# Kernel tuning notes

Measured on AMD Instinct MI355X. Metric: run time of the kernel, lower is better.

The kernel has to match this reference:

```python
import jax, jax.numpy as jnp
import numpy as np

DIM = 768
HEADS = 12
HD = DIM // HEADS  # 64
WIN = 14
N = WIN * WIN  # 196
MLP_HID = 3072
EPS = 1e-6
SCALE = HD ** -0.5


def _ln(x, g, b):
    m = jnp.mean(x, axis=-1, keepdims=True)
    v = jnp.mean(jnp.square(x - m), axis=-1, keepdims=True)
    return (x - m) * jax.lax.rsqrt(v + EPS) * g + b


def _rel_table(rel):
    coords = jnp.arange(WIN)[:, None] - jnp.arange(WIN)[None, :] + (WIN - 1)
    return rel[coords]


def _window_partition(x, ws):
    B, H, W, C = x.shape
    pad_h = (ws - H % ws) % ws
    pad_w = (ws - W % ws) % ws
    x = jnp.pad(x, ((0, 0), (0, pad_h), (0, pad_w), (0, 0)))
    Hp, Wp = H + pad_h, W + pad_w
    x = x.reshape(B, Hp // ws, ws, Wp // ws, ws, C)
    win = x.transpose(0, 1, 3, 2, 4, 5).reshape(-1, ws, ws, C)
    return win, (Hp, Wp)


def _window_unpartition(win, ws, pad_hw, hw):
    Hp, Wp = pad_hw
    H, W = hw
    B = win.shape[0] // (Hp * Wp // ws // ws)
    x = win.reshape(B, Hp // ws, Wp // ws, ws, ws, -1)
    x = x.transpose(0, 1, 3, 2, 4, 5).reshape(B, Hp, Wp, -1)
    return x[:, :H, :W, :]


def _attention(x, qkv_w, qkv_b, proj_w, proj_b, rel_pos_h, rel_pos_w):
    Bw = x.shape[0]
    qkv = x.reshape(Bw, N, DIM) @ qkv_w + qkv_b  # (Bw, N, 3*DIM)
    qkv = qkv.reshape(Bw, N, 3, HEADS, HD).transpose(2, 0, 3, 1, 4)
    qkv = qkv.reshape(3, Bw * HEADS, N, HD)
    q, k, v = qkv[0], qkv[1], qkv[2]
    attn = jnp.einsum('bnd,bmd->bnm', q * SCALE, k)  # (Bw*H, N, N)
    Rh = _rel_table(rel_pos_h)
    Rw = _rel_table(rel_pos_w)
    r_q = q.reshape(-1, WIN, WIN, HD)
    rel_h = jnp.einsum('bhwc,hkc->bhwk', r_q, Rh)
    rel_w = jnp.einsum('bhwc,wkc->bhwk', r_q, Rw)
    attn = (attn.reshape(-1, WIN, WIN, WIN, WIN)
            + rel_h[:, :, :, :, None]
            + rel_w[:, :, :, None, :]).reshape(-1, N, N)
    attn = jax.nn.softmax(attn, axis=-1)
    out = jnp.einsum('bnm,bmd->bnd', attn, v)
    out = out.reshape(Bw, HEADS, WIN, WIN, HD).transpose(0, 2, 3, 1, 4)
    out = out.reshape(Bw, WIN, WIN, DIM)
    return out @ proj_w + proj_b


def setup_inputs() -> dict:
    key = jax.random.key(0)
    ks = jax.random.split(key, 10)
    s = 0.02
    return {
        'x': jax.random.normal(ks[0], (2, 64, 64, DIM), jnp.float32),
        'ln1_g': jnp.ones((DIM,), jnp.float32),
        'ln1_b': jnp.zeros((DIM,), jnp.float32),
        'qkv_w': jax.random.normal(ks[1], (DIM, 3 * DIM), jnp.float32) * s,
        'qkv_b': jax.random.normal(ks[2], (3 * DIM,), jnp.float32) * s,
        'proj_w': jax.random.normal(ks[3], (DIM, DIM), jnp.float32) * s,
        'proj_b': jax.random.normal(ks[4], (DIM,), jnp.float32) * s,
        'rel_pos_h': jax.random.normal(ks[5], (2 * WIN - 1, HD), jnp.float32) * s,
        'rel_pos_w': jax.random.normal(ks[6], (2 * WIN - 1, HD), jnp.float32) * s,
        'ln2_g': jnp.ones((DIM,), jnp.float32),
        'ln2_b': jnp.zeros((DIM,), jnp.float32),
        'fc1_w': jax.random.normal(ks[7], (DIM, MLP_HID), jnp.float32) * s,
        'fc1_b': jnp.zeros((MLP_HID,), jnp.float32),
        'fc2_w': jax.random.normal(ks[8], (MLP_HID, DIM), jnp.float32) * s,
        'fc2_b': jnp.zeros((DIM,), jnp.float32),
    }


def reference(x, ln1_g, ln1_b, qkv_w, qkv_b, proj_w, proj_b,
              rel_pos_h, rel_pos_w, ln2_g, ln2_b, fc1_w, fc1_b, fc2_w, fc2_b):
    B, H, W, _ = x.shape
    shortcut = x
    h = _ln(x, ln1_g, ln1_b)
    win, pad_hw = _window_partition(h, WIN)
    win = _attention(win, qkv_w, qkv_b, proj_w, proj_b, rel_pos_h, rel_pos_w)
    h = _window_unpartition(win, WIN, pad_hw, (H, W))
    x = shortcut + h  # drop_path prob 0 -> identity
    h = _ln(x, ln2_g, ln2_b)
    h = jax.nn.gelu(h @ fc1_w + fc1_b, approximate=False) @ fc2_w + fc2_b
    return x + h
```

## Files before the change

kernel.cpp:

```cpp
#include <hip/hip_runtime.h>
#include <hip/hip_bf16.h>
#include <math.h>


#define DIMC 768
#define HEADS 12
#define WIN 14
#define NTOK 196
#define NWIN 50
#define MROWS 9800
#define YROWS 8192
#define MLP_HID 3072

using bf16x8 = __attribute__((ext_vector_type(8))) short;
using f32x4  = __attribute__((ext_vector_type(4))) float;

__device__ __forceinline__ float bf2f(unsigned short u) {
    return __uint_as_float(((unsigned)u) << 16);
}
__device__ __forceinline__ unsigned short f2bf(float f) {
    unsigned u = __float_as_uint(f);
    unsigned r = (u + 0x7fffu + ((u >> 16) & 1u)) >> 16;
    return (unsigned short)r;
}
__device__ __forceinline__ void gl2lds16(const unsigned short* g, unsigned short* l) {
    __builtin_amdgcn_global_load_lds(
        (const __attribute__((address_space(1))) void*)g,
        (__attribute__((address_space(3))) void*)l, 16, 0, 0);
}

__global__ __launch_bounds__(256) void transpose_w(
        const float* __restrict__ W, unsigned short* __restrict__ Wt,
        int K, int N) {
    __shared__ float t[64][65];
    int k0 = blockIdx.y << 6, n0 = blockIdx.x << 6;
    int tn = threadIdx.x & 63;
    int tk = threadIdx.x >> 6;
    #pragma unroll
    for (int r = 0; r < 16; r++) {
        int k = tk + r * 4;
        t[k][tn] = W[(size_t)(k0 + k) * N + n0 + tn];
    }
    __syncthreads();
    #pragma unroll
    for (int r = 0; r < 16; r++) {
        int n = tk + r * 4;
        Wt[(size_t)(n0 + n) * K + k0 + tn] = f2bf(t[tn][n]);
    }
}

__global__ __launch_bounds__(256) void ln1_win_kernel(
        const float* __restrict__ x, const float* __restrict__ g,
        const float* __restrict__ b, unsigned short* __restrict__ h1) {
    int tid = threadIdx.x;
    int row = blockIdx.x * 4 + (tid >> 6);
    int lane = tid & 63;
    if (row >= MROWS) return;
    int w = row / NTOK, t = row % NTOK;
    int bi = w / 25, wr = w % 25;
    int gy = (wr / 5) * WIN + t / WIN;
    int gx = (wr % 5) * WIN + t % WIN;
    unsigned short* out = h1 + (size_t)row * DIMC;
    if (gy >= 64 || gx >= 64) {
        #pragma unroll
        for (int j = 0; j < 12; j++) out[lane + 64 * j] = 0;
        return;
    }
    const float* xr = x + ((size_t)((bi * 64 + gy) * 64 + gx)) * DIMC;
    float v[12], s = 0.f;
    #pragma unroll
    for (int j = 0; j < 12; j++) { v[j] = xr[lane + 64 * j]; s += v[j]; }
    #pragma unroll
    for (int o = 32; o > 0; o >>= 1) s += __shfl_xor(s, o);
    float mean = s * (1.f / 768.f);
    float q = 0.f;
    #pragma unroll
    for (int j = 0; j < 12; j++) { float d = v[j] - mean; q += d * d; }
    #pragma unroll
    for (int o = 32; o > 0; o >>= 1) q += __shfl_xor(q, o);
    float inv = rsqrtf(q * (1.f / 768.f) + 1e-6f);
    #pragma unroll
    for (int j = 0; j < 12; j++) {
        int c = lane + 64 * j;
        out[c] = f2bf((v[j] - mean) * inv * g[c] + b[c]);
    }
}

__global__ __launch_bounds__(256) void ln2_kernel(
        const float* __restrict__ y, const float* __restrict__ g,
        const float* __restrict__ b, unsigned short* __restrict__ h2) {
    int tid = threadIdx.x;
    int row = blockIdx.x * 4 + (tid >> 6);
    int lane = tid & 63;
    const float* xr = y + (size_t)row * DIMC;
    float v[12], s = 0.f;
    #pragma unroll
    for (int j = 0; j < 12; j++) { v[j] = xr[lane + 64 * j]; s += v[j]; }
    #pragma unroll
    for (int o = 32; o > 0; o >>= 1) s += __shfl_xor(s, o);
    float mean = s * (1.f / 768.f);
    float q = 0.f;
    #pragma unroll
    for (int j = 0; j < 12; j++) { float d = v[j] - mean; q += d * d; }
    #pragma unroll
    for (int o = 32; o > 0; o >>= 1) q += __shfl_xor(q, o);
    float inv = rsqrtf(q * (1.f / 768.f) + 1e-6f);
    unsigned short* out = h2 + (size_t)row * DIMC;
    #pragma unroll
    for (int j = 0; j < 12; j++) {
        int c = lane + 64 * j;
        out[c] = f2bf((v[j] - mean) * inv * g[c] + b[c]);
    }
}

__global__ __launch_bounds__(256) void build_aug(
        const unsigned short* __restrict__ qkvb,
        const float* __restrict__ relph, const float* __restrict__ relpw,
        unsigned short* __restrict__ Aaug, unsigned short* __restrict__ Vt) {
    __shared__ unsigned short qs[208 * 72];
    __shared__ unsigned short rt[64 * 72];
    int tid = threadIdx.x;
    int bh = blockIdx.x, w = bh / HEADS, head = bh % HEADS;
    int lane = tid & 63, wave = tid >> 6;
    int l15 = lane & 15, q4 = lane >> 4, q8 = q4 * 8;
    size_t base = (size_t)w * NTOK * 2304 + head * 64;
    unsigned short* ab = Aaug + (size_t)bh * 256 * 96;

    for (int e = tid; e < 196 * 8; e += 256) {
        int t = e >> 3, s8 = (e & 7) * 8;
        bf16x8 qv = *(const bf16x8*)&qkvb[base + (size_t)t * 2304 + s8];
        *(bf16x8*)&qs[t * 72 + s8] = qv;
        *(bf16x8*)&ab[t * 96 + s8] = qv;
    }
    for (int e = tid; e < 12 * 8; e += 256) {
        bf16x8 z = {};
        *(bf16x8*)&qs[(196 + (e >> 3)) * 72 + (e & 7) * 8] = z;
    }
    for (int e = tid; e < 64 * 8; e += 256) {
        int r = e >> 3, s8 = (e & 7) * 8;
        bf16x8 ov = {};
        if (r < 54) {
            const float* src = (r < 27 ? relph + (size_t)r * 64
                                       : relpw + (size_t)(r - 27) * 64) + s8;
            #pragma unroll
            for (int jj = 0; jj < 8; jj++) ov[jj] = (short)f2bf(src[jj]);
        }
        *(bf16x8*)&rt[r * 72 + s8] = ov;
    }
    for (int e = tid; e < 60 * 12; e += 256) {
        bf16x8 z = {};
        *(bf16x8*)&ab[(size_t)(196 + e / 12) * 96 + (e % 12) * 8] = z;
    }
    for (int e = tid; e < 196; e += 256) {
        ab[e * 96 + 92] = 0; ab[e * 96 + 93] = 0;
        ab[e * 96 + 94] = 0; ab[e * 96 + 95] = 0;
    }
    __syncthreads();

    #pragma unroll
    for (int t = 0; t < 4; t++) {
        int it = wave * 4 + t;
        if (it >= 13) break;
        bf16x8 a0 = *(bf16x8*)&qs[(it * 16 + l15) * 72 + q8];
        bf16x8 a1 = *(bf16x8*)&qs[(it * 16 + l15) * 72 + 32 + q8];
        #pragma unroll
        for (int rt4 = 0; rt4 < 4; rt4++) {
            bf16x8 b0 = *(bf16x8*)&rt[(rt4 * 16 + l15) * 72 + q8];
            bf16x8 b1 = *(bf16x8*)&rt[(rt4 * 16 + l15) * 72 + 32 + q8];
            f32x4 d4 = {};
            d4 = __builtin_amdgcn_mfma_f32_16x16x32_bf16(a0, b0, d4, 0, 0, 0);
            d4 = __builtin_amdgcn_mfma_f32_16x16x32_bf16(a1, b1, d4, 0, 0, 0);
            int rcol = rt4 * 16 + l15;
            #pragma unroll
            for (int r = 0; r < 4; r++) {
                int i = it * 16 + q4 * 4 + r;
                if (i < 196 && rcol < 54) {
                    if (rcol < 27) {
                        int c = 13 + i / 14 - rcol;
                        if (c >= 0 && c < 14) ab[i * 96 + 64 + c] = f2bf(d4[r]);
                    } else {
                        int c = 13 + i % 14 - (rcol - 27);
                        if (c >= 0 && c < 14) ab[i * 96 + 78 + c] = f2bf(d4[r]);
                    }
                }
            }
        }
    }

    unsigned short* vtb = Vt + (size_t)bh * 64 * 224;
    for (int e = tid; e < 196 * 8; e += 256) {
        int j = e >> 3, dg = (e & 7) * 8;
        bf16x8 vv = *(const bf16x8*)&qkvb[base + 1536 + (size_t)j * 2304 + dg];
        #pragma unroll
        for (int k = 0; k < 8; k++)
            vtb[(size_t)(dg + k) * 224 + j] = (unsigned short)vv[k];
    }
    for (int e = tid; e < 64 * 28; e += 256)
        vtb[(size_t)(e / 28) * 224 + 196 + (e % 28)] = 0;
}

__global__ __launch_bounds__(256) void attn_mfma(
        const unsigned short* __restrict__ qkvb,
        const unsigned short* __restrict__ Aaug,
        const unsigned short* __restrict__ Vt,
        unsigned short* __restrict__ out) {
    __shared__ unsigned short Kls[208 * 96];
    __shared__ unsigned short Pls[4][64 * 40];
    int tid = threadIdx.x;
    int bh = blockIdx.x, w = bh / HEADS, head = bh % HEADS;
    int wave = tid >> 6, lane = tid & 63;
    int l15 = lane & 15, q4 = lane >> 4, q8 = q4 * 8;
    size_t kbase = (size_t)w * NTOK * 2304 + head * 64 + 768;
    for (int e = tid; e < 196 * 8; e += 256) {
        int t = e >> 3, s8 = (e & 7) * 8;
        bf16x8 kv = *(const bf16x8*)&qkvb[kbase + (size_t)t * 2304 + s8];
        bf16x8 ko;
        #pragma unroll
        for (int jj = 0; jj < 8; jj++)
            ko[jj] = (short)f2bf(bf2f((unsigned short)kv[jj]) * 0.125f);
        *(bf16x8*)&Kls[t * 96 + s8] = ko;
    }
    bf16x8 z8 = {};
    for (int e = tid; e < 208 * 4; e += 256)
        *(bf16x8*)&Kls[(e >> 2) * 96 + 64 + (e & 3) * 8] = z8;
    for (int e = tid; e < 12 * 8; e += 256)
        *(bf16x8*)&Kls[(196 + (e >> 3)) * 96 + (e & 7) * 8] = z8;
    __syncthreads();
    for (int e = tid; e < 196; e += 256) {
        Kls[e * 96 + 64 + e / WIN] = 0x3F80;
        Kls[e * 96 + 78 + e % WIN] = 0x3F80;
    }
    bf16x8 af[4][3];
    const unsigned short* abse = Aaug + (size_t)bh * 256 * 96;
    #pragma unroll
    for (int it = 0; it < 4; it++)
        #pragma unroll
        for (int c = 0; c < 3; c++)
            af[it][c] = *(const bf16x8*)&abse[(size_t)(wave * 64 + it * 16 + l15) * 96 + c * 32 + q8];
    __syncthreads();

    const unsigned short* vtb = Vt + (size_t)bh * 64 * 224;
    f32x4 o[4][4] = {};
    float lacc[4][4] = {{0.f}};
    bf16x8 bv[4];
    #pragma unroll
    for (int dt = 0; dt < 4; dt++)
        bv[dt] = *(const bf16x8*)&vtb[(dt * 16 + l15) * 224 + q8];

    for (int jp = 0; jp < 7; jp++) {
        f32x4 s[4][2] = {};
        #pragma unroll
        for (int half = 0; half < 2; half++) {
            int jt = jp * 2 + half;
            if (jt < 13) {
                #pragma unroll
                for (int c = 0; c < 3; c++) {
                    bf16x8 bk = *(bf16x8*)&Kls[(jt * 16 + l15) * 96 + c * 32 + q8];
                    #pragma unroll
                    for (int it = 0; it < 4; it++)
                        s[it][half] = __builtin_amdgcn_mfma_f32_16x16x32_bf16(
                            af[it][c], bk, s[it][half], 0, 0, 0);
                }
            }
        }
        __syncthreads();
        #pragma unroll
        for (int half = 0; half < 2; half++) {
            int jt = jp * 2 + half;
            bool valid = (jt < 13) && (jt * 16 + l15) < 196;
            #pragma unroll
            for (int it = 0; it < 4; it++)
                #pragma unroll
                for (int r = 0; r < 4; r++) {
                    float p = valid ? __expf(s[it][half][r]) : 0.f;
                    unsigned short pb = f2bf(p);
                    lacc[it][r] += bf2f(pb);
                    Pls[wave][(it * 16 + q4 * 4 + r) * 40 + half * 16 + l15] = pb;
                }
        }
        __syncthreads();
        bf16x8 ap[4];
        #pragma unroll
        for (int it = 0; it < 4; it++)
            ap[it] = *(bf16x8*)&Pls[wave][(it * 16 + l15) * 40 + q8];
        bf16x8 bvn[4];
        if (jp < 6) {
            #pragma unroll
            for (int dt = 0; dt < 4; dt++)
                bvn[dt] = *(const bf16x8*)&vtb[(dt * 16 + l15) * 224 + (jp + 1) * 32 + q8];
        }
        #pragma unroll
        for (int dt = 0; dt < 4; dt++)
            #pragma unroll
            for (int it = 0; it < 4; it++)
                o[it][dt] = __builtin_amdgcn_mfma_f32_16x16x32_bf16(
                    ap[it], bv[dt], o[it][dt], 0, 0, 0);
        if (jp < 6) {
            #pragma unroll
            for (int dt = 0; dt < 4; dt++) bv[dt] = bvn[dt];
        }
    }
    #pragma unroll
    for (int it = 0; it < 4; it++)
        #pragma unroll
        for (int r = 0; r < 4; r++) {
            float v = lacc[it][r];
            v += __shfl_xor(v, 1); v += __shfl_xor(v, 2);
            v += __shfl_xor(v, 4); v += __shfl_xor(v, 8);
            lacc[it][r] = 1.f / v;
        }
    #pragma unroll
    for (int it = 0; it < 4; it++) {
        int i0 = wave * 64 + it * 16 + q4 * 4;
        #pragma unroll
        for (int r = 0; r < 4; r++) {
            if (i0 + r < 196) {
                size_t rowb = (size_t)(w * NTOK + i0 + r) * DIMC + head * 64;
                #pragma unroll
                for (int dt = 0; dt < 4; dt++)
                    out[rowb + dt * 16 + l15] = f2bf(o[it][dt][r] * lacc[it][r]);
            }
        }
    }
}

template <int EPI>
__global__ __launch_bounds__(256) void mgemm(
        const unsigned short* __restrict__ A, const unsigned short* __restrict__ Bt,
        const float* __restrict__ bias, void* __restrict__ Cout,
        const float* __restrict__ resid, int M, int Nn, int K) {
    __shared__ unsigned short As[128 * 32];
    __shared__ unsigned short Bs[128 * 32];
    int tid = threadIdx.x;
    int lane = tid & 63, wave = tid >> 6;
    int l15 = lane & 15, q8 = (lane >> 4) * 8;
    int m0 = blockIdx.y << 7, n0 = blockIdx.x << 7;
    int wm = (wave >> 1) * 64, wn = (wave & 1) * 64;
    int srow0 = wave * 32 + (lane >> 2);
    int srow1 = srow0 + 16;
    int sseg = (lane & 3) * 8;
    int rmA0 = m0 + srow0; if (rmA0 >= M) rmA0 = M - 1;
    int rmA1 = m0 + srow1; if (rmA1 >= M) rmA1 = M - 1;
    const unsigned short* gA0 = A + (size_t)rmA0 * K + sseg;
    const unsigned short* gA1 = A + (size_t)rmA1 * K + sseg;
    const unsigned short* gB0 = Bt + (size_t)(n0 + srow0) * K + sseg;
    const unsigned short* gB1 = Bt + (size_t)(n0 + srow1) * K + sseg;
    unsigned short* lA0 = As + wave * 1024 + lane * 8;
    unsigned short* lA1 = lA0 + 512;
    unsigned short* lB0 = Bs + wave * 1024 + lane * 8;
    unsigned short* lB1 = lB0 + 512;
    f32x4 acc[4][4] = {};
    for (int k0 = 0; k0 < K; k0 += 32) {
        gl2lds16(gA0 + k0, lA0);
        gl2lds16(gA1 + k0, lA1);
        gl2lds16(gB0 + k0, lB0);
        gl2lds16(gB1 + k0, lB1);
        __syncthreads();
        bf16x8 bfr[4];
        #pragma unroll
        for (int ni = 0; ni < 4; ni++)
            bfr[ni] = *(bf16x8*)&Bs[(wn + ni * 16 + l15) * 32 + q8];
        #pragma unroll
        for (int mi = 0; mi < 4; mi++) {
            bf16x8 afr = *(bf16x8*)&As[(wm + mi * 16 + l15) * 32 + q8];
            #pragma unroll
            for (int ni = 0; ni < 4; ni++)
                acc[mi][ni] = __builtin_amdgcn_mfma_f32_16x16x32_bf16(
                    afr, bfr[ni], acc[mi][ni], 0, 0, 0);
        }
        __syncthreads();
    }
    int q4r = (lane >> 4) * 4;
    #pragma unroll
    for (int mi = 0; mi < 4; mi++) {
        #pragma unroll
        for (int r = 0; r < 4; r++) {
            int row = m0 + wm + mi * 16 + q4r + r;
            if (row >= M) continue;
            if (EPI == 2) {
                int w = row / NTOK, t = row % NTOK;
                int bi = w / 25, wr = w % 25;
                int gy = (wr / 5) * WIN + t / WIN;
                int gx = (wr % 5) * WIN + t % WIN;
                if (gy >= 64 || gx >= 64) continue;
                size_t orow = ((size_t)((bi * 64 + gy) * 64 + gx)) * DIMC;
                #pragma unroll
                for (int ni = 0; ni < 4; ni++) {
                    int col = n0 + wn + ni * 16 + l15;
                    float v = acc[mi][ni][r] + bias[col];
                    ((float*)Cout)[orow + col] = resid[orow + col] + v;
                }
            } else {
                #pragma unroll
                for (int ni = 0; ni < 4; ni++) {
                    int col = n0 + wn + ni * 16 + l15;
                    float v = acc[mi][ni][r] + bias[col];
                    if (EPI == 0) {
                        ((unsigned short*)Cout)[(size_t)row * Nn + col] = f2bf(v);
                    } else if (EPI == 1) {
                        v = 0.5f * v * (1.f + erff(v * 0.70710678118654752f));
                        ((unsigned short*)Cout)[(size_t)row * Nn + col] = f2bf(v);
                    } else {
                        ((float*)Cout)[(size_t)row * Nn + col] =
                            resid[(size_t)row * Nn + col] + v;
                    }
                }
            }
        }
    }
}

extern "C" void kernel_launch(void* const* d_in, const int* in_sizes, int n_in,
                              void* d_out, int out_size, void* d_ws, size_t ws_size,
                              hipStream_t stream) {
    const float* x      = (const float*)d_in[0];
    const float* ln1_g  = (const float*)d_in[1];
    const float* ln1_b  = (const float*)d_in[2];
    const float* qkv_w  = (const float*)d_in[3];
    const float* qkv_b  = (const float*)d_in[4];
    const float* proj_w = (const float*)d_in[5];
    const float* proj_b = (const float*)d_in[6];
    const float* rel_h  = (const float*)d_in[7];
    const float* rel_w  = (const float*)d_in[8];
    const float* ln2_g  = (const float*)d_in[9];
    const float* ln2_b  = (const float*)d_in[10];
    const float* fc1_w  = (const float*)d_in[11];
    const float* fc1_b  = (const float*)d_in[12];
    const float* fc2_w  = (const float*)d_in[13];
    const float* fc2_b  = (const float*)d_in[14];
    float* out = (float*)d_out;
    char* ws = (char*)d_ws;

    unsigned short* wt_qkv  = (unsigned short*)(ws);
    unsigned short* wt_proj = (unsigned short*)(ws + 3538944);
    unsigned short* wt_fc1  = (unsigned short*)(ws + 4718592);
    unsigned short* wt_fc2  = (unsigned short*)(ws + 9437184);
    unsigned short* qkvb    = (unsigned short*)(ws + 14155776);
    float*          yb      = (float*)        (ws + 14155776);
    unsigned short* h2      = (unsigned short*)(ws + 39321600);
    unsigned short* h1      = (unsigned short*)(ws + 59314176);
    unsigned short* attn_o  = h1;
    unsigned short* zb      = h1;
    unsigned short* Aaug    = (unsigned short*)(ws + 74366976);
    unsigned short* Vt      = (unsigned short*)(ws + 103858176);

    transpose_w<<<dim3(36, 12), 256, 0, stream>>>(qkv_w,  wt_qkv,  768, 2304);
    transpose_w<<<dim3(12, 12), 256, 0, stream>>>(proj_w, wt_proj, 768, 768);
    transpose_w<<<dim3(48, 12), 256, 0, stream>>>(fc1_w,  wt_fc1,  768, 3072);
    transpose_w<<<dim3(12, 48), 256, 0, stream>>>(fc2_w,  wt_fc2,  3072, 768);

    ln1_win_kernel<<<(MROWS + 3) / 4, 256, 0, stream>>>(x, ln1_g, ln1_b, h1);

    mgemm<0><<<dim3(18, 77), 256, 0, stream>>>(
        h1, wt_qkv, qkv_b, qkvb, nullptr, MROWS, 2304, DIMC);

    build_aug<<<NWIN * HEADS, 256, 0, stream>>>(qkvb, rel_h, rel_w, Aaug, Vt);

    attn_mfma<<<NWIN * HEADS, 256, 0, stream>>>(qkvb, Aaug, Vt, attn_o);

    mgemm<2><<<dim3(6, 77), 256, 0, stream>>>(
        attn_o, wt_proj, proj_b, yb, x, MROWS, DIMC, DIMC);

    ln2_kernel<<<YROWS / 4, 256, 0, stream>>>(yb, ln2_g, ln2_b, h2);

    mgemm<1><<<dim3(24, 64), 256, 0, stream>>>(
        h2, wt_fc1, fc1_b, zb, nullptr, YROWS, MLP_HID, DIMC);

    mgemm<3><<<dim3(6, 64), 256, 0, stream>>>(
        zb, wt_fc2, fc2_b, out, yb, YROWS, DIMC, MLP_HID);
}
```

Baseline: 474.4 us.

## Add grouped block swizzle and narrower N tiles for projection and fc2 GEMMs

The GEMM kernel now takes a 1D grid and remaps block IDs into groups of 8 M-tiles, so neighbouring blocks share A rows and B columns in L2. The N tile width becomes a template parameter. The projection and fc2 GEMMs use 64-wide N tiles, which doubles their block count from 462/384 to 924/768 and fills more CUs. The trade-off is less reuse per block and more redundant A loads for the narrow-tile GEMMs.

```diff
diff --git a/kernel.cpp b/kernel.cpp
--- a/kernel.cpp
+++ b/kernel.cpp
@@ -324,18 +324,28 @@
     }
 }
 
-template <int EPI>
+template <int EPI, int BN>
 __global__ __launch_bounds__(256) void mgemm(
         const unsigned short* __restrict__ A, const unsigned short* __restrict__ Bt,
         const float* __restrict__ bias, void* __restrict__ Cout,
-        const float* __restrict__ resid, int M, int Nn, int K) {
+        const float* __restrict__ resid, int M, int Nn, int K,
+        int nbx, int nby) {
+    const int NI = BN / 32;
     __shared__ unsigned short As[128 * 32];
-    __shared__ unsigned short Bs[128 * 32];
+    __shared__ unsigned short Bs[BN * 32];
     int tid = threadIdx.x;
     int lane = tid & 63, wave = tid >> 6;
     int l15 = lane & 15, q8 = (lane >> 4) * 8;
-    int m0 = blockIdx.y << 7, n0 = blockIdx.x << 7;
-    int wm = (wave >> 1) * 64, wn = (wave & 1) * 64;
+    int id = blockIdx.x;
+    int per = nbx * 8;
+    int s = id / per;
+    int rem = id - s * per;
+    int rmax = nby - s * 8; if (rmax > 8) rmax = 8;
+    int bx = rem / rmax;
+    int r_ = rem - bx * rmax;
+    int by = s * 8 + r_;
+    int m0 = by << 7, n0 = bx * BN;
+    int wm = (wave >> 1) * 64, wn = (wave & 1) * (BN / 2);
     int srow0 = wave * 32 + (lane >> 2);
     int srow1 = srow0 + 16;
     int sseg = (lane & 3) * 8;
@@ -343,28 +353,29 @@
     int rmA1 = m0 + srow1; if (rmA1 >= M) rmA1 = M - 1;
     const unsigned short* gA0 = A + (size_t)rmA0 * K + sseg;
     const unsigned short* gA1 = A + (size_t)rmA1 * K + sseg;
-    const unsigned short* gB0 = Bt + (size_t)(n0 + srow0) * K + sseg;
-    const unsigned short* gB1 = Bt + (size_t)(n0 + srow1) * K + sseg;
     unsigned short* lA0 = As + wave * 1024 + lane * 8;
     unsigned short* lA1 = lA0 + 512;
-    unsigned short* lB0 = Bs + wave * 1024 + lane * 8;
+    int browB = (BN == 128) ? srow0 : (wave * 16 + (lane >> 2));
+    const unsigned short* gB0 = Bt + (size_t)(n0 + browB) * K + sseg;
+    const unsigned short* gB1 = Bt + (size_t)(n0 + srow1) * K + sseg;
+    unsigned short* lB0 = Bs + ((BN == 128) ? wave * 1024 : wave * 512) + lane * 8;
     unsigned short* lB1 = lB0 + 512;
-    f32x4 acc[4][4] = {};
+    f32x4 acc[4][NI] = {};
     for (int k0 = 0; k0 < K; k0 += 32) {
         gl2lds16(gA0 + k0, lA0);
         gl2lds16(gA1 + k0, lA1);
         gl2lds16(gB0 + k0, lB0);
-        gl2lds16(gB1 + k0, lB1);
+        if (BN == 128) gl2lds16(gB1 + k0, lB1);
         __syncthreads();
-        bf16x8 bfr[4];
-        #pragma unroll
-        for (int ni = 0; ni < 4; ni++)
+        bf16x8 bfr[NI];
+        #pragma unroll
+        for (int ni = 0; ni < NI; ni++)
             bfr[ni] = *(bf16x8*)&Bs[(wn + ni * 16 + l15) * 32 + q8];
         #pragma unroll
         for (int mi = 0; mi < 4; mi++) {
             bf16x8 afr = *(bf16x8*)&As[(wm + mi * 16 + l15) * 32 + q8];
             #pragma unroll
-            for (int ni = 0; ni < 4; ni++)
+            for (int ni = 0; ni < NI; ni++)
                 acc[mi][ni] = __builtin_amdgcn_mfma_f32_16x16x32_bf16(
                     afr, bfr[ni], acc[mi][ni], 0, 0, 0);
         }
@@ -385,14 +396,14 @@
                 if (gy >= 64 || gx >= 64) continue;
                 size_t orow = ((size_t)((bi * 64 + gy) * 64 + gx)) * DIMC;
                 #pragma unroll
-                for (int ni = 0; ni < 4; ni++) {
+                for (int ni = 0; ni < NI; ni++) {
                     int col = n0 + wn + ni * 16 + l15;
                     float v = acc[mi][ni][r] + bias[col];
                     ((float*)Cout)[orow + col] = resid[orow + col] + v;
                 }
             } else {
                 #pragma unroll
-                for (int ni = 0; ni < 4; ni++) {
+                for (int ni = 0; ni < NI; ni++) {
                     int col = n0 + wn + ni * 16 + l15;
                     float v = acc[mi][ni][r] + bias[col];
                     if (EPI == 0) {
@@ -451,21 +462,21 @@
 
     ln1_win_kernel<<<(MROWS + 3) / 4, 256, 0, stream>>>(x, ln1_g, ln1_b, h1);
 
-    mgemm<0><<<dim3(18, 77), 256, 0, stream>>>(
-        h1, wt_qkv, qkv_b, qkvb, nullptr, MROWS, 2304, DIMC);
+    mgemm<0, 128><<<18 * 77, 256, 0, stream>>>(
+        h1, wt_qkv, qkv_b, qkvb, nullptr, MROWS, 2304, DIMC, 18, 77);
 
     build_aug<<<NWIN * HEADS, 256, 0, stream>>>(qkvb, rel_h, rel_w, Aaug, Vt);
 
     attn_mfma<<<NWIN * HEADS, 256, 0, stream>>>(qkvb, Aaug, Vt, attn_o);
 
-    mgemm<2><<<dim3(6, 77), 256, 0, stream>>>(
-        attn_o, wt_proj, proj_b, yb, x, MROWS, DIMC, DIMC);
+    mgemm<2, 64><<<12 * 77, 256, 0, stream>>>(
+        attn_o, wt_proj, proj_b, yb, x, MROWS, DIMC, DIMC, 12, 77);
 
     ln2_kernel<<<YROWS / 4, 256, 0, stream>>>(yb, ln2_g, ln2_b, h2);
 
-    mgemm<1><<<dim3(24, 64), 256, 0, stream>>>(
-        h2, wt_fc1, fc1_b, zb, nullptr, YROWS, MLP_HID, DIMC);
-
-    mgemm<3><<<dim3(6, 64), 256, 0, stream>>>(
-        zb, wt_fc2, fc2_b, out, yb, YROWS, DIMC, MLP_HID);
-}
+    mgemm<1, 128><<<24 * 64, 256, 0, stream>>>(
+        h2, wt_fc1, fc1_b, zb, nullptr, YROWS, MLP_HID, DIMC, 24, 64);
+
+    mgemm<3, 64><<<12 * 64, 256, 0, stream>>>(
+        zb, wt_fc2, fc2_b, out, yb, YROWS, DIMC, MLP_HID, 12, 64);
+}
```

Measured after the change: 452.0 us. 1.05x faster.
